# Kernel optimization log

Hardware: AMD Instinct MI355X
Metric: run time of the kernel (lower is better)

The kernel has to match this reference:

```python
import jax, jax.numpy as jnp
import numpy as np

# Module hyperparameters (from init_kwargs)
H, F = 8, 32            # num_heads, attention_filters
RY, RX = 3, 3           # spatial_radius
PH, PW = 2 * RY + 1, 2 * RX + 1
S = PH * PW             # patch_size = 49
HF = H * F


def setup_inputs() -> dict:
    key = jax.random.key(0)
    ks = jax.random.split(key, 6)
    B, Y, X, C = 4, 64, 64, 256
    x = jax.random.normal(ks[0], (B, Y, X, C), jnp.float32)
    # 1x1 conv kernels == dense matrices over the channel dim (no bias)
    Wq = jax.random.normal(ks[1], (C, HF), jnp.float32) / np.sqrt(C)
    Wk = jax.random.normal(ks[2], (C, HF), jnp.float32) / np.sqrt(C)
    Wv = jax.random.normal(ks[3], (C, HF), jnp.float32) / np.sqrt(C)
    Wo = jax.random.normal(ks[4], (HF, C), jnp.float32) / np.sqrt(HF)
    pos_emb = jax.random.normal(ks[5], (S, HF), jnp.float32) * 0.02
    return {"x": x, "Wq": Wq, "Wk": Wk, "Wv": Wv, "Wo": Wo, "pos_emb": pos_emb}


def reference(x, Wq, Wk, Wv, Wo, pos_emb):
    B, Y, X, C = x.shape
    dtype = x.dtype
    # 1x1 conv projections
    Q = x @ Wq                       # (B,Y,X,HF)
    K = x @ Wk
    V = x @ Wv
    # clipped patch centers (borders reuse interior patches)
    cy = jnp.clip(jnp.arange(Y), RY, Y - RY - 1)   # (Y,)
    cx = jnp.clip(jnp.arange(X), RX, X - RX - 1)   # (X,)
    # query relative-position indices within its patch
    qy = jnp.arange(Y) - cy + RY
    qx = jnp.arange(X) - cx + RX
    qidx = qy[:, None] * PW + qx[None, :]          # (Y,X) in [0,S)
    Q = Q + pos_emb[qidx]                          # add query pos embedding (HF)
    Q = Q.reshape(B, Y, X, H, F)
    K = K.reshape(B, Y, X, H, F)
    V = V.reshape(B, Y, X, H, F)
    cy_g, cx_g = jnp.meshgrid(cy, cx, indexing="ij")  # (Y,X)
    scale = jnp.asarray(1.0 / np.sqrt(F), dtype)
    NEG = jnp.asarray(-1e9, dtype)
    m = jnp.full((B, Y, X, H, 1), NEG, dtype)      # running max
    l = jnp.zeros((B, Y, X, H, 1), dtype)          # running sum-exp
    acc = jnp.zeros((B, Y, X, H, F), dtype)        # running value accumulator
    dy_vec = np.arange(-RY, RY + 1)                # within-chunk offsets ('col' mode)
    for dx in range(-RX, RX + 1):                  # chunk loop over columns (7 chunks)
        ny = jnp.clip(cy_g[None, :, :] + dy_vec[:, None, None], 0, Y - 1)  # (PH,Y,X)
        nx = jnp.clip(cx_g[None, :, :] + dx, 0, X - 1)                     # (1,Y,X)
        nx = jnp.broadcast_to(nx, ny.shape)
        sidx = (dy_vec + RY) * PW + (dx + RX)      # (PH,) relative-pos indices
        # gather neighbor K/V: (B,PH,Y,X,H,F)
        Kc = K[:, ny, nx] + pos_emb[sidx].reshape(PH, 1, 1, H, F)
        Vc = V[:, ny, nx]
        sc = jnp.einsum("byxhf,bsyxhf->byxhs", Q, Kc) * scale  # (B,Y,X,H,PH)
        new_m = jnp.maximum(m, sc.max(axis=-1, keepdims=True))
        alpha = jnp.exp(m - new_m)
        p = jnp.exp(sc - new_m)
        l = l * alpha + p.sum(axis=-1, keepdims=True)
        acc = acc * alpha + jnp.einsum("byxhs,bsyxhf->byxhf", p, Vc)
        m = new_m
    out = (acc / (l + 1e-8)).reshape(B, Y, X, HF) @ Wo
    return out
```

## Files before the change

### kernel.cpp

```cpp
#include <hip/hip_runtime.h>
#include <hip/hip_bf16.h>

static constexpr int NPOS = 4 * 64 * 64;
static constexpr int CD   = 256;
#define QSCALE (0.17677669529663687f * 1.4426950408889634f)

typedef __attribute__((ext_vector_type(8))) short bf16x8;
typedef __attribute__((ext_vector_type(4))) float f32x4;

__device__ __forceinline__ float bflo(unsigned int u) { return __uint_as_float(u << 16); }
__device__ __forceinline__ float bfhi(unsigned int u) { return __uint_as_float(u & 0xffff0000u); }

__device__ __forceinline__ unsigned short bfbits(float f) {
    union { __hip_bfloat16 h; unsigned short u; } cv;
    cv.h = __float2bfloat16(f);
    return cv.u;
}
__device__ __forceinline__ unsigned int packbf2(float lo, float hi) {
    union { __hip_bfloat162 h; unsigned int u; } cv;
    cv.h.x = __float2bfloat16(lo);
    cv.h.y = __float2bfloat16(hi);
    return cv.u;
}
__device__ __forceinline__ uint4 pack8(float4 a, float4 b) {
    uint4 u;
    u.x = packbf2(a.x, a.y); u.y = packbf2(a.z, a.w);
    u.z = packbf2(b.x, b.y); u.w = packbf2(b.z, b.w);
    return u;
}
template<int CTRL>
__device__ __forceinline__ float dpp_mov(float v) {
    return __int_as_float(
        __builtin_amdgcn_update_dpp(0, __float_as_int(v), CTRL, 0xF, 0xF, true));
}
template<int IMM>
__device__ __forceinline__ float swz(float v) {
    return __int_as_float(__builtin_amdgcn_ds_swizzle(__float_as_int(v), IMM));
}

__global__ __launch_bounds__(256) void convert1_kernel(
    const float* __restrict__ Wq, const float* __restrict__ Wk,
    const float* __restrict__ Wv, const float* __restrict__ pe,
    __hip_bfloat16* __restrict__ Wfrag,
    __hip_bfloat16* __restrict__ pebf)
{
    int t = blockIdx.x * 256 + threadIdx.x;
    if (t < 24576) {
        int L = t & 63, ng = (t >> 6) & 7, s = (t >> 9) & 7, T = t >> 12;
        int mat = T >> 1;
        const float* src = (mat == 0) ? Wq : (mat == 1) ? Wk : Wv;
        int ncol  = (T & 1) * 128 + ng * 16 + (L & 15);
        int kbase = s * 32 + (L >> 4) * 8;
        __hip_bfloat16* dst = Wfrag + ((size_t)((T * 8 + s) * 8 + ng) * 64 + L) * 8;
#pragma unroll
        for (int j = 0; j < 8; ++j)
            dst[j] = __float2bfloat16(src[(kbase + j) * 256 + ncol]);
    } else if (t < 24576 + 2048) {
        int u = t - 24576;
        int L = u & 63, Tn = (u >> 6) & 3, h = u >> 8;
        int s = Tn * 16 + (L & 15);
        int kbase = (L >> 4) * 8;
        __hip_bfloat16* dst = pebf + ((size_t)((h * 4 + Tn) * 64 + L)) * 8;
#pragma unroll
        for (int j = 0; j < 8; ++j) {
            float v = (s < 49) ? pe[s * 256 + h * 32 + kbase + j] * QSCALE : 0.f;
            dst[j] = __float2bfloat16(v);
        }
    }
}

__global__ __launch_bounds__(256) void convert2_kernel(
    const float* __restrict__ Wo,
    __hip_bfloat16* __restrict__ Wofrag)
{
    int u = blockIdx.x * 256 + threadIdx.x;
    int L = u & 63, ng = (u >> 6) & 7, s = (u >> 9) & 7, T = (u >> 12) & 1;
    int ncol  = T * 128 + ng * 16 + (L & 15);
    int kbase = s * 32 + (L >> 4) * 8;
    __hip_bfloat16* dst = Wofrag + ((size_t)((T * 8 + s) * 8 + ng) * 64 + L) * 8;
#pragma unroll
    for (int j = 0; j < 8; ++j)
        dst[j] = __float2bfloat16(Wo[(kbase + j) * 256 + ncol]);
}

__global__ __launch_bounds__(256, 4) void qkv_mfma(
    const float* __restrict__ x,
    const __hip_bfloat16* __restrict__ Wfrag,
    const float* __restrict__ pe,
    unsigned short* __restrict__ QA,
    unsigned short* __restrict__ Kd,
    unsigned short* __restrict__ Vt)
{
    __shared__ __align__(16) short As[2][64 * 32];
    const int t = threadIdx.x;
    const int rowbase = blockIdx.x * 64;
    const int g = blockIdx.y;
    const int L = t & 63;
    const int wave = t >> 6;
    const int quad = L >> 4, lrow = L & 15;
    const int T = g * 2 + (wave >> 1);
    const int ngb = (wave & 1) * 4;

    f32x4 acc[4][4];
#pragma unroll
    for (int i = 0; i < 4; ++i)
#pragma unroll
        for (int j = 0; j < 4; ++j) acc[i][j] = (f32x4){0.f, 0.f, 0.f, 0.f};

    const int r_st = t >> 2;
    const float* xsrc = x + (size_t)(rowbase + r_st) * CD + (t & 3) * 8;
    const int ai = r_st * 4 + (t & 3);

    float4 t0 = ((const float4*)xsrc)[0];
    float4 t1 = ((const float4*)xsrc)[1];
    ((uint4*)As[0])[ai] = pack8(t0, t1);
    float4 p00 = ((const float4*)(xsrc + 32))[0];
    float4 p01 = ((const float4*)(xsrc + 32))[1];
    float4 p10 = ((const float4*)(xsrc + 64))[0];
    float4 p11 = ((const float4*)(xsrc + 64))[1];
    __syncthreads();

#pragma unroll
    for (int s = 0; s < 8; ++s) {
        bf16x8 bf[4];
#pragma unroll
        for (int j = 0; j < 4; ++j)
            bf[j] = *(const bf16x8*)(Wfrag +
                     ((size_t)((T * 8 + s) * 8 + ngb + j) * 64 + L) * 8);
        if (s < 7) {
            if (s & 1) {
                ((uint4*)As[(s + 1) & 1])[ai] = pack8(p10, p11);
                if (s + 3 < 8) {
                    p10 = ((const float4*)(xsrc + (s + 3) * 32))[0];
                    p11 = ((const float4*)(xsrc + (s + 3) * 32))[1];
                }
            } else {
                ((uint4*)As[(s + 1) & 1])[ai] = pack8(p00, p01);
                if (s + 3 < 8) {
                    p00 = ((const float4*)(xsrc + (s + 3) * 32))[0];
                    p01 = ((const float4*)(xsrc + (s + 3) * 32))[1];
                }
            }
        }
        const short* Ab = As[s & 1];
#pragma unroll
        for (int i = 0; i < 4; ++i) {
            bf16x8 af = *(const bf16x8*)(Ab + (i * 16 + lrow) * 32 + quad * 8);
#pragma unroll
            for (int j = 0; j < 4; ++j)
                acc[i][j] = __builtin_amdgcn_mfma_f32_16x16x32_bf16(af, bf[j], acc[i][j], 0, 0, 0);
        }
        __syncthreads();
    }

#pragma unroll
    for (int i = 0; i < 4; ++i) {
#pragma unroll
        for (int r = 0; r < 4; ++r) {
            int row = rowbase + i * 16 + quad * 4 + r;
            if (g == 0) {
                int yy = (row >> 6) & 63, xx = row & 63;
                int cy = min(max(yy, 3), 60), cx = min(max(xx, 3), 60);
                int qidx = (yy - cy + 3) * 7 + (xx - cx + 3);
#pragma unroll
                for (int j = 0; j < 4; ++j) {
                    int c = wave * 64 + j * 16 + lrow;
                    QA[(size_t)row * CD + c] = bfbits(acc[i][j][r] + pe[qidx * 256 + c]);
                }
            } else if (g == 1) {
#pragma unroll
                for (int j = 0; j < 4; ++j) {
                    int c = wave * 64 + j * 16 + lrow;
                    Kd[(size_t)row * CD + c] = bfbits(acc[i][j][r] * QSCALE);
                }
            } else {
#pragma unroll
                for (int j = 0; j < 4; ++j) {
                    int c = wave * 64 + j * 16 + lrow;
                    Vt[(size_t)c * 16384 + row + 3] = bfbits(acc[i][j][r]);
                }
            }
        }
    }
}

__global__ __launch_bounds__(256) void attn_mfma(
    unsigned short* QA,
    const unsigned short* __restrict__ Kd,
    const unsigned short* __restrict__ Vt,
    const __hip_bfloat16* __restrict__ pebf)
{
    __shared__ float qpes[4][16 * 64];
    __shared__ __align__(16) unsigned short ps[4][16 * 40];
    const int t = threadIdx.x, w = t >> 6, L = t & 63;
    const int lrow = L & 15, quad = L >> 4;
    const int id = blockIdx.x * 4 + w;
    const int tile = id >> 3, h = id & 7;
    const int pos0 = tile * 16;
    const int x0 = pos0 & 63;
    const int yy = (pos0 >> 6) & 63, bb = pos0 >> 12;
    const int cy = min(max(yy, 3), 60);

    int cxr[4];
#pragma unroll
    for (int r = 0; r < 4; ++r)
        cxr[r] = min(max(x0 + quad * 4 + r, 3), 60) - x0;

    const int kc0 = min(max(x0 - 3 + lrow, 0), 63);
    const int kc1 = min(max(x0 + 13 + lrow, 0), 63);

    const bf16x8 qa = *(const bf16x8*)(QA + (size_t)(pos0 + lrow) * 256 + h * 32 + quad * 8);

    float* qp = qpes[w];
    const f32x4 zero = {0.f, 0.f, 0.f, 0.f};
#pragma unroll
    for (int Tn = 0; Tn < 4; ++Tn) {
        bf16x8 bp = *(const bf16x8*)(pebf + ((size_t)((h * 4 + Tn) * 64 + L)) * 8);
        f32x4 c = __builtin_amdgcn_mfma_f32_16x16x32_bf16(qa, bp, zero, 0, 0, 0);
#pragma unroll
        for (int r = 0; r < 4; ++r)
            qp[(quad * 4 + r) * 64 + Tn * 16 + lrow] = c[r];
    }
    __builtin_amdgcn_s_waitcnt(0xc07f);

    float lacc[4] = {0.f, 0.f, 0.f, 0.f};
    f32x4 o0 = zero, o1 = zero;
    unsigned short* pw = ps[w];
    int rowpos = bb * 4096 + (cy - 3) * 64;

    for (int dy = 0; dy < 7; ++dy, rowpos += 64) {
        const bf16x8 bk0 = *(const bf16x8*)(Kd + (size_t)(rowpos + kc0) * 256 + h * 32 + quad * 8);
        const bf16x8 bk1 = *(const bf16x8*)(Kd + (size_t)(rowpos + kc1) * 256 + h * 32 + quad * 8);
        f32x4 sc0 = __builtin_amdgcn_mfma_f32_16x16x32_bf16(qa, bk0, zero, 0, 0, 0);
        f32x4 sc1 = __builtin_amdgcn_mfma_f32_16x16x32_bf16(qa, bk1, zero, 0, 0, 0);
        const int dy7 = dy * 7;
#pragma unroll
        for (int r = 0; r < 4; ++r) {
            const int i = quad * 4 + r;
            {
                int dx3 = lrow - cxr[r];
                float qpe = qp[i * 64 + dy7 + min(max(dx3, 0), 6)];
                float e = exp2f(sc0[r] + qpe);
                float p = ((unsigned)dx3 <= 6u) ? e : 0.f;
                lacc[r] += p;
                pw[i * 40 + lrow] = bfbits(p);
            }
            {
                int dx3 = 16 + lrow - cxr[r];
                float qpe = qp[i * 64 + dy7 + min(max(dx3, 0), 6)];
                float e = exp2f(sc1[r] + qpe);
                float p = ((unsigned)dx3 <= 6u) ? e : 0.f;
                lacc[r] += p;
                pw[i * 40 + 16 + lrow] = bfbits(p);
            }
        }
        __builtin_amdgcn_s_waitcnt(0xc07f);
        const bf16x8 pa = *(const bf16x8*)(pw + lrow * 40 + quad * 8);
        const bf16x8 bv0 = *(const bf16x8*)(Vt + (size_t)(h * 32 + lrow) * 16384 + rowpos + x0 + quad * 8);
        const bf16x8 bv1 = *(const bf16x8*)(Vt + (size_t)(h * 32 + 16 + lrow) * 16384 + rowpos + x0 + quad * 8);
        o0 = __builtin_amdgcn_mfma_f32_16x16x32_bf16(pa, bv0, o0, 0, 0, 0);
        o1 = __builtin_amdgcn_mfma_f32_16x16x32_bf16(pa, bv1, o1, 0, 0, 0);
    }

#pragma unroll
    for (int r = 0; r < 4; ++r) {
        float v = lacc[r];
        v += dpp_mov<0xB1>(v);
        v += dpp_mov<0x4E>(v);
        v += swz<0x101F>(v);
        v += swz<0x201F>(v);
        const float inv = 1.f / (v + 1e-8f);
        const int row = pos0 + quad * 4 + r;
        QA[(size_t)row * 256 + h * 32 + lrow]      = bfbits(o0[r] * inv);
        QA[(size_t)row * 256 + h * 32 + 16 + lrow] = bfbits(o1[r] * inv);
    }
}

__global__ __launch_bounds__(256, 4) void oproj_mfma(
    const unsigned int* __restrict__ A,
    const __hip_bfloat16* __restrict__ Wofrag,
    float* __restrict__ out)
{
    __shared__ __align__(16) short As[2][64 * 32];
    const int t = threadIdx.x;
    const int rowbase = blockIdx.x * 64;
    const int L = t & 63;
    const int wave = t >> 6;
    const int quad = L >> 4, lrow = L & 15;
    const int T = wave >> 1;
    const int ngb = (wave & 1) * 4;

    f32x4 acc[4][4];
#pragma unroll
    for (int i = 0; i < 4; ++i)
#pragma unroll
        for (int j = 0; j < 4; ++j) acc[i][j] = (f32x4){0.f, 0.f, 0.f, 0.f};

    const int r_st = t >> 2;
    const uint4* asrc = (const uint4*)A + (size_t)(rowbase + r_st) * 32 + (t & 3);
    const int ai = r_st * 4 + (t & 3);

    ((uint4*)As[0])[ai] = asrc[0];
    uint4 pf0 = asrc[4];
    uint4 pf1 = asrc[8];
    __syncthreads();

#pragma unroll
    for (int s = 0; s < 8; ++s) {
        bf16x8 bf[4];
#pragma unroll
        for (int j = 0; j < 4; ++j)
            bf[j] = *(const bf16x8*)(Wofrag +
                     ((size_t)((T * 8 + s) * 8 + ngb + j) * 64 + L) * 8);
        if (s < 7) {
            if (s & 1) {
                ((uint4*)As[(s + 1) & 1])[ai] = pf1;
                if (s + 3 < 8) pf1 = asrc[(s + 3) * 4];
            } else {
                ((uint4*)As[(s + 1) & 1])[ai] = pf0;
                if (s + 3 < 8) pf0 = asrc[(s + 3) * 4];
            }
        }
        const short* Ab = As[s & 1];
#pragma unroll
        for (int i = 0; i < 4; ++i) {
            bf16x8 af = *(const bf16x8*)(Ab + (i * 16 + lrow) * 32 + quad * 8);
#pragma unroll
            for (int j = 0; j < 4; ++j)
                acc[i][j] = __builtin_amdgcn_mfma_f32_16x16x32_bf16(af, bf[j], acc[i][j], 0, 0, 0);
        }
        __syncthreads();
    }

#pragma unroll
    for (int i = 0; i < 4; ++i)
#pragma unroll
        for (int r = 0; r < 4; ++r) {
            int row = rowbase + i * 16 + quad * 4 + r;
#pragma unroll
            for (int j = 0; j < 4; ++j) {
                int c = wave * 64 + j * 16 + lrow;
                out[(size_t)row * CD + c] = acc[i][j][r];
            }
        }
}

extern "C" void kernel_launch(void* const* d_in, const int* in_sizes, int n_in,
                              void* d_out, int out_size, void* d_ws, size_t ws_size,
                              hipStream_t stream)
{
    const float* x  = (const float*)d_in[0];
    const float* Wq = (const float*)d_in[1];
    const float* Wk = (const float*)d_in[2];
    const float* Wv = (const float*)d_in[3];
    const float* Wo = (const float*)d_in[4];
    const float* pe = (const float*)d_in[5];
    float* out = (float*)d_out;

    char* ws  = (char*)d_ws;
    char* dob = (char*)d_out;
    unsigned short* QA = (unsigned short*)ws;
    unsigned short* Kd = (unsigned short*)(ws + (8u << 20));
    __hip_bfloat16* Wofrag = (__hip_bfloat16*)(ws + (8u << 20));
    unsigned short* Vt = (unsigned short*)dob;
    __hip_bfloat16* Wfrag = (__hip_bfloat16*)(dob + (8u << 20) + 4096);
    __hip_bfloat16* pebf  = (__hip_bfloat16*)(dob + (8u << 20) + 4096 + (384u << 10));

    convert1_kernel<<<104, 256, 0, stream>>>(Wq, Wk, Wv, pe, Wfrag, pebf);
    qkv_mfma<<<dim3(256, 3), 256, 0, stream>>>(x, Wfrag, pe, QA, Kd, Vt);
    attn_mfma<<<2048, 256, 0, stream>>>(QA, Kd, Vt, pebf);
    convert2_kernel<<<32, 256, 0, stream>>>(Wo, Wofrag);
    oproj_mfma<<<256, 256, 0, stream>>>((const unsigned int*)QA, Wofrag, out);
}
```

Baseline: 139.4 us.

## Pre-convert x to bf16, stage GEMM tiles via async global-to-LDS loads

Adds a kernel that converts x to bf16 once, so the QKV GEMM (launched with three column groups) no longer reads and packs fp32 x three times. Both GEMMs now stage A tiles with global_load_lds async copies instead of register prefetch plus LDS stores. The Wo fragment conversion is folded into convert1, dropping one launch. The output-projection tile is halved to 32 rows so it runs twice as many blocks. The trade-offs are an extra pass over x, a single-stage prefetch with less latency hiding than the old two-ahead register scheme, and a reworked workspace layout.

```diff
diff --git a/kernel.cpp b/kernel.cpp
--- a/kernel.cpp
+++ b/kernel.cpp
@@ -37,12 +37,28 @@
 __device__ __forceinline__ float swz(float v) {
     return __int_as_float(__builtin_amdgcn_ds_swizzle(__float_as_int(v), IMM));
 }
+__device__ __forceinline__ void async16(void* lds, const void* g) {
+    __builtin_amdgcn_global_load_lds(
+        (const __attribute__((address_space(1))) unsigned int*)g,
+        (__attribute__((address_space(3))) unsigned int*)lds, 16, 0, 0);
+}
+
+__global__ __launch_bounds__(256) void convertx_kernel(
+    const float* __restrict__ x, unsigned short* __restrict__ xb)
+{
+    int t = blockIdx.x * 256 + threadIdx.x;
+    const float4* s = (const float4*)x + (size_t)t * 2;
+    float4 a = s[0], b = s[1];
+    ((uint4*)xb)[t] = pack8(a, b);
+}
 
 __global__ __launch_bounds__(256) void convert1_kernel(
     const float* __restrict__ Wq, const float* __restrict__ Wk,
-    const float* __restrict__ Wv, const float* __restrict__ pe,
+    const float* __restrict__ Wv, const float* __restrict__ Wo,
+    const float* __restrict__ pe,
     __hip_bfloat16* __restrict__ Wfrag,
-    __hip_bfloat16* __restrict__ pebf)
+    __hip_bfloat16* __restrict__ pebf,
+    __hip_bfloat16* __restrict__ Wofrag)
 {
     int t = blockIdx.x * 256 + threadIdx.x;
     if (t < 24576) {
@@ -55,7 +71,7 @@
 #pragma unroll
         for (int j = 0; j < 8; ++j)
             dst[j] = __float2bfloat16(src[(kbase + j) * 256 + ncol]);
-    } else if (t < 24576 + 2048) {
+    } else if (t < 26624) {
         int u = t - 24576;
         int L = u & 63, Tn = (u >> 6) & 3, h = u >> 8;
         int s = Tn * 16 + (L & 15);
@@ -66,25 +82,20 @@
             float v = (s < 49) ? pe[s * 256 + h * 32 + kbase + j] * QSCALE : 0.f;
             dst[j] = __float2bfloat16(v);
         }
-    }
-}
-
-__global__ __launch_bounds__(256) void convert2_kernel(
-    const float* __restrict__ Wo,
-    __hip_bfloat16* __restrict__ Wofrag)
-{
-    int u = blockIdx.x * 256 + threadIdx.x;
-    int L = u & 63, ng = (u >> 6) & 7, s = (u >> 9) & 7, T = (u >> 12) & 1;
-    int ncol  = T * 128 + ng * 16 + (L & 15);
-    int kbase = s * 32 + (L >> 4) * 8;
-    __hip_bfloat16* dst = Wofrag + ((size_t)((T * 8 + s) * 8 + ng) * 64 + L) * 8;
-#pragma unroll
-    for (int j = 0; j < 8; ++j)
-        dst[j] = __float2bfloat16(Wo[(kbase + j) * 256 + ncol]);
+    } else if (t < 34816) {
+        int u = t - 26624;
+        int L = u & 63, ng = (u >> 6) & 7, s = (u >> 9) & 7, T = (u >> 12) & 1;
+        int ncol  = T * 128 + ng * 16 + (L & 15);
+        int kbase = s * 32 + (L >> 4) * 8;
+        __hip_bfloat16* dst = Wofrag + ((size_t)((T * 8 + s) * 8 + ng) * 64 + L) * 8;
+#pragma unroll
+        for (int j = 0; j < 8; ++j)
+            dst[j] = __float2bfloat16(Wo[(kbase + j) * 256 + ncol]);
+    }
 }
 
 __global__ __launch_bounds__(256, 4) void qkv_mfma(
-    const float* __restrict__ x,
+    const unsigned short* __restrict__ xb,
     const __hip_bfloat16* __restrict__ Wfrag,
     const float* __restrict__ pe,
     unsigned short* __restrict__ QA,
@@ -107,48 +118,28 @@
 #pragma unroll
         for (int j = 0; j < 4; ++j) acc[i][j] = (f32x4){0.f, 0.f, 0.f, 0.f};
 
-    const int r_st = t >> 2;
-    const float* xsrc = x + (size_t)(rowbase + r_st) * CD + (t & 3) * 8;
-    const int ai = r_st * 4 + (t & 3);
-
-    float4 t0 = ((const float4*)xsrc)[0];
-    float4 t1 = ((const float4*)xsrc)[1];
-    ((uint4*)As[0])[ai] = pack8(t0, t1);
-    float4 p00 = ((const float4*)(xsrc + 32))[0];
-    float4 p01 = ((const float4*)(xsrc + 32))[1];
-    float4 p10 = ((const float4*)(xsrc + 64))[0];
-    float4 p11 = ((const float4*)(xsrc + 64))[1];
+    const unsigned short* xs = xb + (size_t)(rowbase + (t >> 2)) * CD + (t & 3) * 8;
+    short* d0 = &As[0][t * 8];
+    short* d1 = &As[1][t * 8];
+
+    async16(d0, xs);
     __syncthreads();
 
 #pragma unroll
     for (int s = 0; s < 8; ++s) {
-        bf16x8 bf[4];
+        if (s < 7) async16((s & 1) ? d0 : d1, xs + (s + 1) * 32);
+        bf16x8 bfr[4];
 #pragma unroll
         for (int j = 0; j < 4; ++j)
-            bf[j] = *(const bf16x8*)(Wfrag +
-                     ((size_t)((T * 8 + s) * 8 + ngb + j) * 64 + L) * 8);
-        if (s < 7) {
-            if (s & 1) {
-                ((uint4*)As[(s + 1) & 1])[ai] = pack8(p10, p11);
-                if (s + 3 < 8) {
-                    p10 = ((const float4*)(xsrc + (s + 3) * 32))[0];
-                    p11 = ((const float4*)(xsrc + (s + 3) * 32))[1];
-                }
-            } else {
-                ((uint4*)As[(s + 1) & 1])[ai] = pack8(p00, p01);
-                if (s + 3 < 8) {
-                    p00 = ((const float4*)(xsrc + (s + 3) * 32))[0];
-                    p01 = ((const float4*)(xsrc + (s + 3) * 32))[1];
-                }
-            }
-        }
+            bfr[j] = *(const bf16x8*)(Wfrag +
+                      ((size_t)((T * 8 + s) * 8 + ngb + j) * 64 + L) * 8);
         const short* Ab = As[s & 1];
 #pragma unroll
         for (int i = 0; i < 4; ++i) {
             bf16x8 af = *(const bf16x8*)(Ab + (i * 16 + lrow) * 32 + quad * 8);
 #pragma unroll
             for (int j = 0; j < 4; ++j)
-                acc[i][j] = __builtin_amdgcn_mfma_f32_16x16x32_bf16(af, bf[j], acc[i][j], 0, 0, 0);
+                acc[i][j] = __builtin_amdgcn_mfma_f32_16x16x32_bf16(af, bfr[j], acc[i][j], 0, 0, 0);
         }
         __syncthreads();
     }
@@ -277,63 +268,53 @@
 }
 
 __global__ __launch_bounds__(256, 4) void oproj_mfma(
-    const unsigned int* __restrict__ A,
+    const unsigned short* __restrict__ A,
     const __hip_bfloat16* __restrict__ Wofrag,
     float* __restrict__ out)
 {
-    __shared__ __align__(16) short As[2][64 * 32];
+    __shared__ __align__(16) short As[2][32 * 32];
     const int t = threadIdx.x;
-    const int rowbase = blockIdx.x * 64;
+    const int rowbase = blockIdx.x * 32;
     const int L = t & 63;
     const int wave = t >> 6;
     const int quad = L >> 4, lrow = L & 15;
     const int T = wave >> 1;
     const int ngb = (wave & 1) * 4;
 
-    f32x4 acc[4][4];
-#pragma unroll
-    for (int i = 0; i < 4; ++i)
+    f32x4 acc[2][4];
+#pragma unroll
+    for (int i = 0; i < 2; ++i)
 #pragma unroll
         for (int j = 0; j < 4; ++j) acc[i][j] = (f32x4){0.f, 0.f, 0.f, 0.f};
 
-    const int r_st = t >> 2;
-    const uint4* asrc = (const uint4*)A + (size_t)(rowbase + r_st) * 32 + (t & 3);
-    const int ai = r_st * 4 + (t & 3);
-
-    ((uint4*)As[0])[ai] = asrc[0];
-    uint4 pf0 = asrc[4];
-    uint4 pf1 = asrc[8];
+    const unsigned short* asrc = A + (size_t)(rowbase + (t >> 2)) * CD + (t & 3) * 8;
+    short* d0 = &As[0][t * 8];
+    short* d1 = &As[1][t * 8];
+
+    if (t < 128) async16(d0, asrc);
     __syncthreads();
 
 #pragma unroll
     for (int s = 0; s < 8; ++s) {
-        bf16x8 bf[4];
+        if (s < 7 && t < 128) async16((s & 1) ? d0 : d1, asrc + (s + 1) * 32);
+        bf16x8 bfr[4];
 #pragma unroll
         for (int j = 0; j < 4; ++j)
-            bf[j] = *(const bf16x8*)(Wofrag +
-                     ((size_t)((T * 8 + s) * 8 + ngb + j) * 64 + L) * 8);
-        if (s < 7) {
-            if (s & 1) {
-                ((uint4*)As[(s + 1) & 1])[ai] = pf1;
-                if (s + 3 < 8) pf1 = asrc[(s + 3) * 4];
-            } else {
-                ((uint4*)As[(s + 1) & 1])[ai] = pf0;
-                if (s + 3 < 8) pf0 = asrc[(s + 3) * 4];
-            }
-        }
+            bfr[j] = *(const bf16x8*)(Wofrag +
+                      ((size_t)((T * 8 + s) * 8 + ngb + j) * 64 + L) * 8);
         const short* Ab = As[s & 1];
 #pragma unroll
-        for (int i = 0; i < 4; ++i) {
+        for (int i = 0; i < 2; ++i) {
             bf16x8 af = *(const bf16x8*)(Ab + (i * 16 + lrow) * 32 + quad * 8);
 #pragma unroll
             for (int j = 0; j < 4; ++j)
-                acc[i][j] = __builtin_amdgcn_mfma_f32_16x16x32_bf16(af, bf[j], acc[i][j], 0, 0, 0);
+                acc[i][j] = __builtin_amdgcn_mfma_f32_16x16x32_bf16(af, bfr[j], acc[i][j], 0, 0, 0);
         }
         __syncthreads();
     }
 
 #pragma unroll
-    for (int i = 0; i < 4; ++i)
+    for (int i = 0; i < 2; ++i)
 #pragma unroll
         for (int r = 0; r < 4; ++r) {
             int row = rowbase + i * 16 + quad * 4 + r;
@@ -357,18 +338,19 @@
     const float* pe = (const float*)d_in[5];
     float* out = (float*)d_out;
 
-    char* ws  = (char*)d_ws;
-    char* dob = (char*)d_out;
+    char* ws = (char*)d_ws;
     unsigned short* QA = (unsigned short*)ws;
     unsigned short* Kd = (unsigned short*)(ws + (8u << 20));
-    __hip_bfloat16* Wofrag = (__hip_bfloat16*)(ws + (8u << 20));
-    unsigned short* Vt = (unsigned short*)dob;
-    __hip_bfloat16* Wfrag = (__hip_bfloat16*)(dob + (8u << 20) + 4096);
-    __hip_bfloat16* pebf  = (__hip_bfloat16*)(dob + (8u << 20) + 4096 + (384u << 10));
-
-    convert1_kernel<<<104, 256, 0, stream>>>(Wq, Wk, Wv, pe, Wfrag, pebf);
-    qkv_mfma<<<dim3(256, 3), 256, 0, stream>>>(x, Wfrag, pe, QA, Kd, Vt);
+    unsigned short* Vt = (unsigned short*)(ws + (16u << 20));
+    unsigned short* xb = (unsigned short*)(ws + (24u << 20) + 4096);
+    char* fr = ws + (32u << 20) + 8192;
+    __hip_bfloat16* Wfrag  = (__hip_bfloat16*)fr;
+    __hip_bfloat16* pebf   = (__hip_bfloat16*)(fr + (384u << 10));
+    __hip_bfloat16* Wofrag = (__hip_bfloat16*)(fr + (416u << 10));
+
+    convertx_kernel<<<2048, 256, 0, stream>>>(x, xb);
+    convert1_kernel<<<136, 256, 0, stream>>>(Wq, Wk, Wv, Wo, pe, Wfrag, pebf, Wofrag);
+    qkv_mfma<<<dim3(256, 3), 256, 0, stream>>>(xb, Wfrag, pe, QA, Kd, Vt);
     attn_mfma<<<2048, 256, 0, stream>>>(QA, Kd, Vt, pebf);
-    convert2_kernel<<<32, 256, 0, stream>>>(Wo, Wofrag);
-    oproj_mfma<<<256, 256, 0, stream>>>((const unsigned int*)QA, Wofrag, out);
-}
+    oproj_mfma<<<512, 256, 0, stream>>>(QA, Wofrag, out);
+}
```

Result: no change. 138.4 us (-0.7%).
